# Optimization experiments

Hardware: AMD Instinct MI355X
Metric: run time of the kernel (lower is better)

Reference implementation:

```python
import jax, jax.numpy as jnp
import numpy as np

B, C, D, H, W = 2, 8, 64, 160, 160


def setup_inputs() -> dict:
    key = jax.random.key(0)
    k1, k2, k3 = jax.random.split(key, 3)
    net_output = jax.random.normal(k1, (B, C, D, H, W), dtype=jnp.float32)
    # sample 0 only contains classes {0..4} (partial labels), sample 1 all 8 classes,
    # so the dynamic task-merging / channel-padding paths are exercised.
    lab0 = jax.random.randint(k2, (1, D, H, W), 0, 5)
    lab1 = jax.random.randint(k3, (1, D, H, W), 0, C)
    labels = jnp.concatenate([lab0, lab1], axis=0)  # [B,D,H,W]
    target = jax.nn.one_hot(labels, C, dtype=jnp.float32).transpose(0, 4, 1, 2, 3)
    return {"net_output": net_output, "target": target}


def reference(net_output, target):
    # Masked (non-compacted) re-expression of DC_CE_Marginal_loss.
    # Original pipeline: partial_onehot compacts target to the per-sample
    # present classes (sorted, background first) and zero-pads to the batch
    # max L; merge_prediction adds logits of absent classes into background;
    # softmax_fun softmaxes each sample over its valid channels only; dice is
    # averaged over valid channels; CE uses full softmax over L channels where
    # the (L - n_i) padding channels carry logit 0 and target 0.  All of this
    # is channel-permutation invariant, so we compute it in the original
    # channel layout with a presence mask and account for the zero-logit
    # padding channels analytically.
    Cc = net_output.shape[1]
    labels = jnp.argmax(target, axis=1)  # [B,D,H,W]
    counts = jax.vmap(lambda l: jnp.bincount(l.ravel(), length=Cc))(labels)  # [B,C]
    present = counts > 0
    pm = present.astype(net_output.dtype)[:, :, None, None, None]  # [B,C,1,1,1]

    # merge_prediction: absent foreground logits folded into background
    bg_extra = jnp.sum(net_output[:, 1:] * (1.0 - pm[:, 1:]), axis=1, keepdims=True)
    m = jnp.concatenate([net_output[:, :1] + bg_extra, net_output[:, 1:]], axis=1)
    t_eff = target * pm  # compacted target (absent channels dropped)

    n = jnp.sum(present, axis=1).astype(net_output.dtype)  # valid channels / sample
    pad = jnp.max(n) - n  # number of zero-logit padding channels / sample

    zm = jnp.where(pm > 0, m, -jnp.inf)  # logits restricted to present classes
    # ---- cross entropy over L = max(n) channels (padding logits are 0) ----
    lse_p = jax.nn.logsumexp(zm, axis=1)  # [B,D,H,W]
    lse = jnp.where((pad > 0)[:, None, None, None],
                    jnp.logaddexp(lse_p, jnp.log(jnp.maximum(pad, 1.0))[:, None, None, None]),
                    lse_p)
    ce_loss = jnp.mean(lse - jnp.sum(t_eff * m, axis=1))

    # ---- dice over per-sample valid channels (softmax over present only) ----
    p = jax.nn.softmax(zm, axis=1)  # absent channels -> 0 (softmax_fun)
    ref_vol = jnp.sum(t_eff, axis=(2, 3, 4))      # [B,C]
    seg_vol = jnp.sum(p, axis=(2, 3, 4))
    intersect = jnp.sum(t_eff * p, axis=(2, 3, 4))
    dice_c = 2.0 * intersect / (ref_vol + seg_vol + 1e-5)
    dice_i = 1.0 - jnp.sum(present * dice_c, axis=1) / n  # mean over valid channels
    dc_loss = jnp.mean(dice_i)

    return 0.5 * ce_loss + 0.5 * dc_loss
```

## Files before the change

### kernel.cpp

```cpp
#include <hip/hip_runtime.h>
#include <math.h>

#define BB 2
#define CC 8
#define DD 64
#define HH 160
#define WW 160
#define SS (DD*HH*WW)
#define NVOX (BB*SS)
#define THREADS 256
#define GPT 2
#define BLOCKS_PER_SAMPLE (SS/(THREADS*4*GPT))
#define NBLOCKS (BB*BLOCKS_PER_SAMPLE)

#define L2E 1.4426950408889634f
#define LN2 0.6931471805599453f

typedef float f32x4 __attribute__((ext_vector_type(4)));

__global__ __launch_bounds__(THREADS)
void pass_label(const f32x4* __restrict__ tgt,
                unsigned short* __restrict__ lab16,
                unsigned int* __restrict__ cnt_part) {
    __shared__ unsigned int scnt[CC];
    const int tid = threadIdx.x;
    if (tid < CC) scnt[tid] = 0u;
    __syncthreads();

    const int b   = blockIdx.x / BLOCKS_PER_SAMPLE;
    const int blk = blockIdx.x % BLOCKS_PER_SAMPLE;
    const int S4  = SS / 4;
    const f32x4* base = tgt + (size_t)b * CC * S4;
    unsigned short* lab = lab16 + (size_t)b * S4;

    for (int it = 0; it < GPT; ++it) {
        const int g = blk * (THREADS * GPT) + it * THREADS + tid;
        f32x4 v[CC];
        #pragma unroll
        for (int c = 0; c < CC; ++c) v[c] = __builtin_nontemporal_load(base + (size_t)c * S4 + g);

        int l0 = 0, l1 = 0, l2 = 0, l3 = 0;
        #pragma unroll
        for (int c = 1; c < CC; ++c) {
            if (v[c][0] > 0.5f) l0 = c;
            if (v[c][1] > 0.5f) l1 = c;
            if (v[c][2] > 0.5f) l2 = c;
            if (v[c][3] > 0.5f) l3 = c;
        }
        lab[g] = (unsigned short)(l0 | (l1 << 4) | (l2 << 8) | (l3 << 12));
        atomicAdd(&scnt[l0], 1u);
        atomicAdd(&scnt[l1], 1u);
        atomicAdd(&scnt[l2], 1u);
        atomicAdd(&scnt[l3], 1u);
    }
    __syncthreads();
    if (tid < CC) cnt_part[tid * NBLOCKS + blockIdx.x] = scnt[tid];
}

__global__ __launch_bounds__(512)
void reduce_counts(const unsigned int* __restrict__ cnt_part,
                   unsigned int* __restrict__ counts,
                   float* __restrict__ fpar) {
    __shared__ unsigned int sc[2 * CC];
    const int tid = threadIdx.x;
    const int w = tid >> 6, lane = tid & 63;
    unsigned int a0 = 0, a1 = 0;
    const unsigned int* col = cnt_part + w * NBLOCKS;
    #pragma unroll
    for (int k = 0; k < NBLOCKS / 64; ++k) {
        const int blk = lane + (k << 6);
        const unsigned int v = col[blk];
        if (blk < BLOCKS_PER_SAMPLE) a0 += v; else a1 += v;
    }
    #pragma unroll
    for (int off = 32; off > 0; off >>= 1) {
        a0 += __shfl_down(a0, off, 64);
        a1 += __shfl_down(a1, off, 64);
    }
    if (lane == 0) { sc[w] = a0; sc[CC + w] = a1; counts[w] = a0; counts[CC + w] = a1; }
    __syncthreads();
    if (tid == 0) {
        int n0 = 0, n1 = 0;
        for (int c = 0; c < CC; ++c) { n0 += (sc[c] > 0u); n1 += (sc[CC + c] > 0u); }
        const int maxn = n0 > n1 ? n0 : n1;
        for (int c = 0; c < CC; ++c) {
            fpar[c]      = (sc[c]      > 0u) ? 0.0f : 1.0f;
            fpar[CC + c] = (sc[CC + c] > 0u) ? 0.0f : 1.0f;
        }
        fpar[16] = (float)(maxn - n0);
        fpar[17] = (float)(maxn - n1);
    }
}

__global__ __launch_bounds__(THREADS)
void pass_main(const f32x4* __restrict__ net,
               const unsigned short* __restrict__ lab16,
               const float* __restrict__ fpar,
               float* __restrict__ part) {
    __shared__ float s_ab[CC];
    __shared__ float s_padf;
    __shared__ float s_red[2 * CC + 1];

    const int tid = threadIdx.x;
    const int b   = blockIdx.x / BLOCKS_PER_SAMPLE;
    const int blk = blockIdx.x % BLOCKS_PER_SAMPLE;

    if (tid < CC) s_ab[tid] = fpar[b * CC + tid];
    if (tid == CC) s_padf = fpar[2 * CC + b];
    if (tid < 2 * CC + 1) s_red[tid] = 0.0f;
    __syncthreads();

    float ab[CC], bias[CC];
    #pragma unroll
    for (int c = 0; c < CC; ++c) { ab[c] = s_ab[c]; bias[c] = -2048.0f * ab[c]; }
    const float padf = s_padf;

    float segA[CC];
    float intA[CC];
    #pragma unroll
    for (int c = 0; c < CC; ++c) { segA[c] = 0.0f; intA[c] = 0.0f; }
    float ceA = 0.0f;

    const int S4 = SS / 4;
    const f32x4* base = net + (size_t)b * CC * S4;
    const unsigned short* lab = lab16 + (size_t)b * S4;

    for (int it = 0; it < GPT; ++it) {
        const int g = blk * (THREADS * GPT) + it * THREADS + tid;
        f32x4 v[CC];
        #pragma unroll
        for (int c = 0; c < CC; ++c) v[c] = __builtin_nontemporal_load(base + (size_t)c * S4 + g);
        const unsigned int Lp = lab[g];

        #pragma unroll
        for (int j = 0; j < 4; ++j) {
            const int lab_j = (Lp >> (4 * j)) & 0xF;
            float m[CC];
            m[0] = v[0][j];
            float f1 = ab[1] * v[1][j];
            float f2 = ab[2] * v[2][j];
            float f3 = ab[3] * v[3][j];
            float f4 = ab[4] * v[4][j];
            float f5 = ab[5] * v[5][j];
            float f6 = ab[6] * v[6][j];
            float f7 = ab[7] * v[7][j];
            #pragma unroll
            for (int c = 1; c < CC; ++c) m[c] = v[c][j];
            m[0] += ((f1 + f2) + (f3 + f4)) + ((f5 + f6) + f7);

            float e[CC];
            #pragma unroll
            for (int c = 0; c < CC; ++c)
                e[c] = __builtin_amdgcn_exp2f(fmaf(m[c], L2E, bias[c]));
            const float sp = ((e[0] + e[1]) + (e[2] + e[3])) + ((e[4] + e[5]) + (e[6] + e[7]));
            const float se = sp + padf;
            const float lse = LN2 * __builtin_amdgcn_logf(se);

            float inv = __builtin_amdgcn_rcpf(sp);
            inv = inv * (2.0f - sp * inv);

            float mlab = 0.0f;
            #pragma unroll
            for (int c = 0; c < CC; ++c) {
                const float p = e[c] * inv;
                segA[c] += p;
                const bool isl = (lab_j == c);
                intA[c] += isl ? p : 0.0f;
                mlab     = isl ? m[c] : mlab;
            }
            ceA += lse - mlab;
        }
    }

    #pragma unroll
    for (int off = 32; off > 0; off >>= 1) {
        #pragma unroll
        for (int c = 0; c < CC; ++c) {
            segA[c] += __shfl_down(segA[c], off, 64);
            intA[c] += __shfl_down(intA[c], off, 64);
        }
        ceA += __shfl_down(ceA, off, 64);
    }
    if ((tid & 63) == 0) {
        #pragma unroll
        for (int c = 0; c < CC; ++c) {
            atomicAdd(&s_red[c],      segA[c]);
            atomicAdd(&s_red[CC + c], intA[c]);
        }
        atomicAdd(&s_red[2 * CC], ceA);
    }
    __syncthreads();
    if (tid < 2 * CC + 1) part[tid * NBLOCKS + blockIdx.x] = s_red[tid];
}

__global__ __launch_bounds__(512)
void finalize(const unsigned int* __restrict__ counts,
              const float* __restrict__ part,
              float* __restrict__ out) {
    __shared__ float sred[2 * CC + 1][2];
    const int tid = threadIdx.x;
    const int w = tid >> 6, lane = tid & 63;
    for (int q = w; q < 2 * CC + 1; q += 8) {
        float a0 = 0.0f, a1 = 0.0f;
        const float* col = part + q * NBLOCKS;
        #pragma unroll
        for (int k = 0; k < NBLOCKS / 64; ++k) {
            const int blk = lane + (k << 6);
            const float v = col[blk];
            if (blk < BLOCKS_PER_SAMPLE) a0 += v; else a1 += v;
        }
        #pragma unroll
        for (int off = 32; off > 0; off >>= 1) {
            a0 += __shfl_down(a0, off, 64);
            a1 += __shfl_down(a1, off, 64);
        }
        if (lane == 0) { sred[q][0] = a0; sred[q][1] = a1; }
    }
    __syncthreads();
    if (tid == 0) {
        const float ce = (sred[2 * CC][0] + sred[2 * CC][1]) / (float)NVOX;
        float dc = 0.0f;
        for (int b = 0; b < BB; ++b) {
            int nb = 0;
            float acc = 0.0f;
            for (int c = 0; c < CC; ++c) {
                const unsigned int cnt = counts[b * CC + c];
                if (cnt > 0u) {
                    ++nb;
                    const float R = (float)cnt;
                    const float Sg = sred[c][b];
                    const float I  = sred[CC + c][b];
                    acc += 2.0f * I / (R + Sg + 1e-5f);
                }
            }
            dc += 1.0f - acc / (float)nb;
        }
        dc /= (float)BB;
        out[0] = 0.5f * ce + 0.5f * dc;
    }
}

extern "C" void kernel_launch(void* const* d_in, const int* in_sizes, int n_in,
                              void* d_out, int out_size, void* d_ws, size_t ws_size,
                              hipStream_t stream) {
    const f32x4* net = (const f32x4*)d_in[0];
    const f32x4* tgt = (const f32x4*)d_in[1];
    float* out = (float*)d_out;

    unsigned int*   counts   = (unsigned int*)d_ws;
    float*          fpar     = (float*)((char*)d_ws + 64);
    unsigned int*   cnt_part = (unsigned int*)((char*)d_ws + 256);
    float*          part     = (float*)((char*)d_ws + 256 + 51200);
    unsigned short* lab16    = (unsigned short*)((char*)d_ws + 256 + 51200 + 108800);

    pass_label<<<NBLOCKS, THREADS, 0, stream>>>(tgt, lab16, cnt_part);
    reduce_counts<<<1, 512, 0, stream>>>(cnt_part, counts, fpar);
    pass_main<<<NBLOCKS, THREADS, 0, stream>>>(net, lab16, fpar, part);
    finalize<<<1, 512, 0, stream>>>(counts, part, out);
}
```

Measured before the change: 46.71 us.

## Fold count reduction into main pass and finalize, double groups per thread

```diff
diff --git a/kernel.cpp b/kernel.cpp
--- a/kernel.cpp
+++ b/kernel.cpp
@@ -9,7 +9,7 @@
 #define SS (DD*HH*WW)
 #define NVOX (BB*SS)
 #define THREADS 256
-#define GPT 2
+#define GPT 4
 #define BLOCKS_PER_SAMPLE (SS/(THREADS*4*GPT))
 #define NBLOCKS (BB*BLOCKS_PER_SAMPLE)
 
@@ -57,63 +57,51 @@
     if (tid < CC) cnt_part[tid * NBLOCKS + blockIdx.x] = scnt[tid];
 }
 
-__global__ __launch_bounds__(512)
-void reduce_counts(const unsigned int* __restrict__ cnt_part,
-                   unsigned int* __restrict__ counts,
-                   float* __restrict__ fpar) {
-    __shared__ unsigned int sc[2 * CC];
-    const int tid = threadIdx.x;
-    const int w = tid >> 6, lane = tid & 63;
-    unsigned int a0 = 0, a1 = 0;
-    const unsigned int* col = cnt_part + w * NBLOCKS;
-    #pragma unroll
-    for (int k = 0; k < NBLOCKS / 64; ++k) {
-        const int blk = lane + (k << 6);
-        const unsigned int v = col[blk];
-        if (blk < BLOCKS_PER_SAMPLE) a0 += v; else a1 += v;
-    }
-    #pragma unroll
-    for (int off = 32; off > 0; off >>= 1) {
-        a0 += __shfl_down(a0, off, 64);
-        a1 += __shfl_down(a1, off, 64);
-    }
-    if (lane == 0) { sc[w] = a0; sc[CC + w] = a1; counts[w] = a0; counts[CC + w] = a1; }
-    __syncthreads();
-    if (tid == 0) {
-        int n0 = 0, n1 = 0;
-        for (int c = 0; c < CC; ++c) { n0 += (sc[c] > 0u); n1 += (sc[CC + c] > 0u); }
-        const int maxn = n0 > n1 ? n0 : n1;
-        for (int c = 0; c < CC; ++c) {
-            fpar[c]      = (sc[c]      > 0u) ? 0.0f : 1.0f;
-            fpar[CC + c] = (sc[CC + c] > 0u) ? 0.0f : 1.0f;
-        }
-        fpar[16] = (float)(maxn - n0);
-        fpar[17] = (float)(maxn - n1);
-    }
-}
-
 __global__ __launch_bounds__(THREADS)
 void pass_main(const f32x4* __restrict__ net,
                const unsigned short* __restrict__ lab16,
-               const float* __restrict__ fpar,
+               const unsigned int* __restrict__ cnt_part,
                float* __restrict__ part) {
-    __shared__ float s_ab[CC];
-    __shared__ float s_padf;
+    __shared__ unsigned int sc[2 * CC];
     __shared__ float s_red[2 * CC + 1];
 
     const int tid = threadIdx.x;
     const int b   = blockIdx.x / BLOCKS_PER_SAMPLE;
     const int blk = blockIdx.x % BLOCKS_PER_SAMPLE;
 
-    if (tid < CC) s_ab[tid] = fpar[b * CC + tid];
-    if (tid == CC) s_padf = fpar[2 * CC + b];
+    {
+        const int w = tid >> 6, lane = tid & 63;
+        const int c   = 2 * w + (lane >> 5);
+        const int sub = lane & 31;
+        const unsigned int* col = cnt_part + c * NBLOCKS;
+        unsigned int a0 = 0, a1 = 0;
+        #pragma unroll
+        for (int i = 0; i < NBLOCKS / 32; ++i) {
+            const int idx = sub + (i << 5);
+            const unsigned int v = col[idx];
+            if (idx < BLOCKS_PER_SAMPLE) a0 += v; else a1 += v;
+        }
+        #pragma unroll
+        for (int off = 16; off > 0; off >>= 1) {
+            a0 += __shfl_down(a0, off, 64);
+            a1 += __shfl_down(a1, off, 64);
+        }
+        if (sub == 0) { sc[c] = a0; sc[CC + c] = a1; }
+    }
     if (tid < 2 * CC + 1) s_red[tid] = 0.0f;
     __syncthreads();
 
+    int n0 = 0, n1 = 0;
+    #pragma unroll
+    for (int c = 0; c < CC; ++c) { n0 += (sc[c] > 0u); n1 += (sc[CC + c] > 0u); }
+    const int maxn = n0 > n1 ? n0 : n1;
+    const float padf = (float)(maxn - ((b == 0) ? n0 : n1));
     float ab[CC], bias[CC];
     #pragma unroll
-    for (int c = 0; c < CC; ++c) { ab[c] = s_ab[c]; bias[c] = -2048.0f * ab[c]; }
-    const float padf = s_padf;
+    for (int c = 0; c < CC; ++c) {
+        ab[c]   = (sc[b * CC + c] > 0u) ? 0.0f : 1.0f;
+        bias[c] = -2048.0f * ab[c];
+    }
 
     float segA[CC];
     float intA[CC];
@@ -194,20 +182,24 @@
 }
 
 __global__ __launch_bounds__(512)
-void finalize(const unsigned int* __restrict__ counts,
+void finalize(const unsigned int* __restrict__ cnt_part,
               const float* __restrict__ part,
               float* __restrict__ out) {
     __shared__ float sred[2 * CC + 1][2];
+    __shared__ unsigned int sc[2 * CC];
     const int tid = threadIdx.x;
     const int w = tid >> 6, lane = tid & 63;
+
     for (int q = w; q < 2 * CC + 1; q += 8) {
         float a0 = 0.0f, a1 = 0.0f;
         const float* col = part + q * NBLOCKS;
         #pragma unroll
-        for (int k = 0; k < NBLOCKS / 64; ++k) {
-            const int blk = lane + (k << 6);
-            const float v = col[blk];
-            if (blk < BLOCKS_PER_SAMPLE) a0 += v; else a1 += v;
+        for (int k = 0; k < 13; ++k) {
+            const int idx = lane + (k << 6);
+            if (idx < NBLOCKS) {
+                const float v = col[idx];
+                if (idx < BLOCKS_PER_SAMPLE) a0 += v; else a1 += v;
+            }
         }
         #pragma unroll
         for (int off = 32; off > 0; off >>= 1) {
@@ -215,6 +207,24 @@
             a1 += __shfl_down(a1, off, 64);
         }
         if (lane == 0) { sred[q][0] = a0; sred[q][1] = a1; }
+    }
+    {
+        unsigned int a0 = 0, a1 = 0;
+        const unsigned int* col = cnt_part + w * NBLOCKS;
+        #pragma unroll
+        for (int k = 0; k < 13; ++k) {
+            const int idx = lane + (k << 6);
+            if (idx < NBLOCKS) {
+                const unsigned int v = col[idx];
+                if (idx < BLOCKS_PER_SAMPLE) a0 += v; else a1 += v;
+            }
+        }
+        #pragma unroll
+        for (int off = 32; off > 0; off >>= 1) {
+            a0 += __shfl_down(a0, off, 64);
+            a1 += __shfl_down(a1, off, 64);
+        }
+        if (lane == 0) { sc[w] = a0; sc[CC + w] = a1; }
     }
     __syncthreads();
     if (tid == 0) {
@@ -224,7 +234,7 @@
             int nb = 0;
             float acc = 0.0f;
             for (int c = 0; c < CC; ++c) {
-                const unsigned int cnt = counts[b * CC + c];
+                const unsigned int cnt = sc[b * CC + c];
                 if (cnt > 0u) {
                     ++nb;
                     const float R = (float)cnt;
@@ -247,14 +257,11 @@
     const f32x4* tgt = (const f32x4*)d_in[1];
     float* out = (float*)d_out;
 
-    unsigned int*   counts   = (unsigned int*)d_ws;
-    float*          fpar     = (float*)((char*)d_ws + 64);
-    unsigned int*   cnt_part = (unsigned int*)((char*)d_ws + 256);
-    float*          part     = (float*)((char*)d_ws + 256 + 51200);
-    unsigned short* lab16    = (unsigned short*)((char*)d_ws + 256 + 51200 + 108800);
+    unsigned int*   cnt_part = (unsigned int*)d_ws;
+    float*          part     = (float*)((char*)d_ws + 25600);
+    unsigned short* lab16    = (unsigned short*)((char*)d_ws + 80000);
 
     pass_label<<<NBLOCKS, THREADS, 0, stream>>>(tgt, lab16, cnt_part);
-    reduce_counts<<<1, 512, 0, stream>>>(cnt_part, counts, fpar);
-    pass_main<<<NBLOCKS, THREADS, 0, stream>>>(net, lab16, fpar, part);
-    finalize<<<1, 512, 0, stream>>>(counts, part, out);
-}
+    pass_main<<<NBLOCKS, THREADS, 0, stream>>>(net, lab16, cnt_part, part);
+    finalize<<<1, 512, 0, stream>>>(cnt_part, part, out);
+}
```

After: 48.42 us. 1.04x slower.
